# Optimization experiments

Measured on AMD Instinct MI355X. Metric: run time of the kernel, lower is better.

## Reference

```python
import jax, jax.numpy as jnp
import numpy as np

COMMITMENT_WEIGHT = 0.25


def _vq_layer(residual, codebook):
    """One euclidean VQ layer: nearest-codeword lookup + straight-through.
    residual: [B,T,D], codebook: [K,D].
    Returns (q_st [B,T,D], idx [B,T], commit_loss scalar).
    """
    B, T, D = residual.shape
    flat = residual.reshape(-1, D)  # [N,D]
    d2 = (jnp.sum(flat * flat, axis=-1, keepdims=True)
          - 2.0 * flat @ codebook.T
          + jnp.sum(codebook * codebook, axis=-1))  # [N,K]
    idx = jnp.argmin(d2, axis=-1)                   # [N]
    q = codebook[idx].reshape(B, T, D)
    # straight-through estimator (as in vector_quantize_pytorch)
    q_st = residual + jax.lax.stop_gradient(q - residual)
    commit_loss = COMMITMENT_WEIGHT * jnp.mean(
        (jax.lax.stop_gradient(q) - residual) ** 2)
    return q_st, idx.reshape(B, T), commit_loss


def setup_inputs() -> dict:
    key = jax.random.key(0)
    ks = jax.random.split(key, 9)
    D = 768
    sizes = [2, 4, 8, 16, 32, 64, 128, 256]
    inp = {"x": jax.random.normal(ks[0], (32, 2048, D), dtype=jnp.float32)}
    for i, K in enumerate(sizes):
        inp[f"cb{i}"] = jax.random.normal(ks[i + 1], (K, D), dtype=jnp.float32)
    return inp


def reference(x, cb0, cb1, cb2, cb3, cb4, cb5, cb6, cb7):
    codebooks = [cb0, cb1, cb2, cb3, cb4, cb5, cb6, cb7]
    residual = x
    quantized = jnp.zeros_like(x)
    all_indices = []
    total_commit_loss = jnp.float32(0.0)
    for cb in codebooks:  # fixed 8 structurally-distinct layers
        q, idx, commit = _vq_layer(residual, cb)
        quantized = quantized + q
        residual = residual - q
        all_indices.append(idx)
        total_commit_loss = total_commit_loss + commit
    all_indices = jnp.stack(all_indices, axis=-1)  # [B,T,num_layers]
    return quantized, all_indices, total_commit_loss
```

## Files before the change

### kernel.cpp

```cpp
#include <hip/hip_runtime.h>
#include <stdint.h>

#define NTOK 65536
#define DIM  768
#define NCB  512
#define NC   510
#define TAU  1.0f

typedef _Float16 f16x8 __attribute__((ext_vector_type(8)));
typedef float f32x4 __attribute__((ext_vector_type(4)));

#define WS_C32   0u
#define WS_CHI   1572864u
#define WS_CNORM 3145728u
#define WS_G     3147776u
#define WS_IDX   4196352u
#define WS_PART  6293504u
#define WS_PART2 6359040u
#define WS_S     8388608u
#define S_BYTES  67108864u

__device__ __forceinline__ void gl_lds16(const void* g, void* l){
  __builtin_amdgcn_global_load_lds(
      (const __attribute__((address_space(1))) unsigned int*)g,
      (__attribute__((address_space(3))) unsigned int*)l,
      16, 0, 0);
}

__global__ void k_prep(const float* __restrict__ cb0, const float* __restrict__ cb1,
                       const float* __restrict__ cb2, const float* __restrict__ cb3,
                       const float* __restrict__ cb4, const float* __restrict__ cb5,
                       const float* __restrict__ cb6, const float* __restrict__ cb7,
                       char* __restrict__ ws){
  const int r = blockIdx.x, t = threadIdx.x;
  const float* srcs[8] = {cb0,cb1,cb2,cb3,cb4,cb5,cb6,cb7};
  const int off[8] = {0,2,6,14,30,62,126,254};
  const int KK[8]  = {2,4,8,16,32,64,128,256};
  const float* src = nullptr;
#pragma unroll
  for (int l=0;l<8;l++)
    if (r >= off[l] && r < off[l]+KK[l]) src = srcs[l] + (size_t)(r - off[l]) * DIM;
  float* C32 = (float*)(ws + WS_C32);
  _Float16* Chi = (_Float16*)(ws + WS_CHI);
  double ss = 0.0;
#pragma unroll
  for (int i=0;i<3;i++){
    const int e = t + i*256;
    const float v = src ? src[e] : 0.f;
    C32[(size_t)r*DIM + e] = v;
    Chi[(size_t)r*DIM + e] = (_Float16)v;
    ss += (double)v * (double)v;
  }
  __shared__ double red[256];
  red[t] = ss; __syncthreads();
  for (int sdown=128; sdown>0; sdown>>=1){
    if (t < sdown) red[t] += red[t+sdown];
    __syncthreads();
  }
  if (t == 0){
    float* cnp = (float*)(ws + WS_CNORM);
    cnp[r] = (r < NC) ? (float)red[0] : 1e30f;
  }
}

__global__ void k_gram(char* __restrict__ ws){
  const int i = blockIdx.x, t = threadIdx.x;
  const float* __restrict__ C32 = (const float*)(ws + WS_C32);
  __shared__ float row[DIM];
  for (int e=t; e<DIM; e+=256) row[e] = C32[(size_t)i*DIM + e];
  __syncthreads();
  float* __restrict__ G = (float*)(ws + WS_G);
  for (int j=t; j<NCB; j+=256){
    const float4* cj = (const float4*)(C32 + (size_t)j*DIM);
    double d = 0.0;
    for (int k=0; k<DIM/4; k++){
      const float4 b = cj[k];
      d += (double)row[4*k]*(double)b.x + (double)row[4*k+1]*(double)b.y
         + (double)row[4*k+2]*(double)b.z + (double)row[4*k+3]*(double)b.w;
    }
    G[(size_t)i*NCB + j] = (float)(2.0*d);
  }
}

__global__ __launch_bounds__(256, 3) void k_gemm(const float* __restrict__ x,
                                                 const char* __restrict__ ws,
                                                 _Float16* __restrict__ Sq,
                                                 float* __restrict__ part2){
  __shared__ __align__(16) char smem[49152];
  const int t = threadIdx.x, lane = t & 63, w = t >> 6;
  const int wm = w >> 1, wn = w & 1;
  const int bid = blockIdx.x;
  const int xcd = bid & 7, jj = bid >> 3;
  const int mt = xcd*64 + (jj >> 2), nt = jj & 3;
  const _Float16* __restrict__ Chi = (const _Float16*)(ws + WS_CHI);
  const float* __restrict__ cn = (const float*)(ws + WS_CNORM);

  f32x4 acc[4][4];
#pragma unroll
  for (int i=0;i<4;i++)
#pragma unroll
    for (int j=0;j<4;j++) acc[i][j] = {0.f,0.f,0.f,0.f};

  float xs = 0.f;

  for (int kt=0; kt<12; kt++){
#pragma unroll
    for (int i8=0;i8<8;i8++){
      const int r0 = w*32 + i8*4;
      const int row = r0 + (lane>>4);
      const int g = lane & 15;
      const int sg = g ^ (((row&7)<<1) | ((row>>3)&1));
      const size_t go = (size_t)(mt*128 + row)*DIM + (size_t)kt*64 + sg*4;
      gl_lds16(x + go, smem + r0*256);
    }
#pragma unroll
    for (int c4=0;c4<4;c4++){
      const int r0 = w*32 + c4*8;
      const int rloc = r0 + (lane>>3);
      const int jsrc = (lane&7) ^ (rloc&7);
      const size_t go = (size_t)(nt*128 + rloc)*DIM + (size_t)kt*64 + jsrc*8;
      gl_lds16(Chi + go, smem + 32768 + r0*128);
    }
    __syncthreads();
    if ((kt & 3) == nt){
#pragma unroll
      for (int g=0; g<8; g++){
        const f32x4 v = *(const f32x4*)(smem + t*128 + g*16);
        xs += v[0]*v[0] + v[1]*v[1] + v[2]*v[2] + v[3]*v[3];
      }
    }
#pragma unroll
    for (int kk=0; kk<2; kk++){
      f16x8 fa[4], fb[4];
#pragma unroll
      for (int mf=0;mf<4;mf++){
        const int m = wm*64 + mf*16 + (lane&15);
        const int maskm = ((m&7)<<1) | ((m>>3)&1);
        const int ch = kk*4 + (lane>>4);
        const int g0 = (2*ch) ^ maskm;
        const f32x4 lo = *(const f32x4*)(smem + m*256 + g0*16);
        const f32x4 hi = *(const f32x4*)(smem + m*256 + (g0^1)*16);
        f16x8 r;
        r[0]=(_Float16)lo[0]; r[1]=(_Float16)lo[1]; r[2]=(_Float16)lo[2]; r[3]=(_Float16)lo[3];
        r[4]=(_Float16)hi[0]; r[5]=(_Float16)hi[1]; r[6]=(_Float16)hi[2]; r[7]=(_Float16)hi[3];
        fa[mf] = r;
      }
#pragma unroll
      for (int nf=0;nf<4;nf++){
        const int c = wn*64 + nf*16 + (lane&15);
        const uint bb = (uint)(32768 + c*128 + ((((kk<<2)+(lane>>4)) ^ (c&7))*16));
        fb[nf] = *(const f16x8*)(smem + bb);
      }
#pragma unroll
      for (int mf=0;mf<4;mf++)
#pragma unroll
        for (int nf=0;nf<4;nf++)
          acc[mf][nf] = __builtin_amdgcn_mfma_f32_16x16x32_f16(fa[mf], fb[nf], acc[mf][nf], 0,0,0);
    }
    __syncthreads();
  }

#pragma unroll
  for (int d=32; d>0; d>>=1) xs += __shfl_down(xs, d);
  if (lane == 0) ((float*)smem)[w] = xs;
  __syncthreads();
  if (t == 0) part2[bid] = ((float*)smem)[0] + ((float*)smem)[1]
                         + ((float*)smem)[2] + ((float*)smem)[3];

#pragma unroll
  for (int mf=0;mf<4;mf++)
#pragma unroll
    for (int nf=0;nf<4;nf++){
      const f32x4 v = acc[mf][nf];
      const int col  = nt*128 + wn*64 + nf*16 + (lane&15);
      const int row0 = mt*128 + wm*64 + mf*16 + ((lane>>4)<<2);
      const float cnc = cn[col];
#pragma unroll
      for (int e=0;e<4;e++)
        Sq[(size_t)(row0+e)*NCB + col] = (_Float16)(cnc - 2.f*v[e] - 768.f);
    }
}

template<int FUSED>
__global__ __launch_bounds__(512, 4) void k_chain(const float* __restrict__ x,
                                                  const _Float16* __restrict__ S,
                                                  char* __restrict__ ws,
                                                  float* __restrict__ out,
                                                  float* __restrict__ part){
  const int t = threadIdx.x, lane = t & 63, w = t >> 6;
  const size_t tok = (size_t)blockIdx.x*8 + w;
  const float* __restrict__ cn  = (const float*)(ws + WS_CNORM);
  const float* __restrict__ G2  = (const float*)(ws + WS_G);
  const float* __restrict__ C32 = (const float*)(ws + WS_C32);

  float sv[8], s0[8];
  {
    const uint* sp = (const uint*)(S + tok*NCB);
#pragma unroll
    for (int j=0;j<4;j++){
      union { uint u; _Float16 h[2]; } cv;
      cv.u = sp[j*64 + lane];
      sv[2*j]   = (float)cv.h[0];
      sv[2*j+1] = (float)cv.h[1];
    }
  }
#pragma unroll
  for (int k=0;k<8;k++) s0[k] = sv[k];

  int mcs[8];
  float tot = 0.f;

#pragma unroll
  for (int l=0; l<8; ++l){
    const int cs = (2<<l) - 2;
    const int ce = cs + (2<<l);
    float sc[8];
    float bv = 3e38f; int bc = 511;
#pragma unroll
    for (int j=0;j<4;j++){
      const int c0 = j*128 + lane*2;
      const float sA = (c0   >= cs && c0   < ce) ? sv[2*j]   : 3e38f;
      const float sB = (c0+1 >= cs && c0+1 < ce) ? sv[2*j+1] : 3e38f;
      sc[2*j] = sA; sc[2*j+1] = sB;
      if (sA < bv){ bv = sA; bc = c0; }
      if (sB < bv){ bv = sB; bc = c0+1; }
    }
    uint u = __float_as_uint(bv);
    u ^= (u & 0x80000000u) ? 0xFFFFFFFFu : 0x80000000u;
    uint key = (u & 0xFFFFFE00u) | ((uint)bc & 511u);
#pragma unroll
    for (int d=1; d<64; d<<=1){
      const uint ok = (uint)__shfl_xor((int)key, d);
      key = (ok < key) ? ok : key;
    }
    const int mc0 = (int)(key & 511u);
    const uint vq = key & 0xFFFFFE00u;
    const uint sb = (vq & 0x80000000u) ? (vq ^ 0x80000000u) : ~vq;
    const float bv_est = __uint_as_float(sb);
    const float thr = bv_est + TAU;

    int bm = 0;
#pragma unroll
    for (int k=0;k<8;k++)
      if (sc[k] <= thr) bm |= 1 << k;
    const unsigned long long lmask = __ballot(bm != 0);
    const int b0 = __ffsll((long long)lmask) - 1;
    const int bm0 = __shfl(bm, b0);
    const bool multi = (__popcll(lmask) > 1) || ((bm0 & (bm0-1)) != 0);

    int mc = mc0;
    float ssel = bv_est + 768.f;
    if (multi){
      float xv[12];
      {
        const float4* xp = (const float4*)(x + tok*DIM + lane*12);
#pragma unroll
        for (int q=0;q<3;q++){
          const float4 v = xp[q];
          xv[q*4]=v.x; xv[q*4+1]=v.y; xv[q*4+2]=v.z; xv[q*4+3]=v.w;
        }
      }
      double bve = 1e300; int bce = 0x7fffffff;
      unsigned long long Lm = lmask;
      while (Lm){
        const int b = __ffsll((long long)Lm) - 1; Lm &= Lm - 1;
        const int mbits = __shfl(bm, b);
#pragma unroll
        for (int k=0;k<8;k++){
          if (mbits & (1<<k)){
            const int c = (k>>1)*128 + b*2 + (k&1);
            const float dkv = __shfl((sv[k] - s0[k]) * 0.5f, b);
            const float* __restrict__ crow = C32 + (size_t)c*DIM + lane*12;
            double dd = 0.0;
#pragma unroll
            for (int q=0;q<3;q++){
              const float4 v = *(const float4*)(crow + q*4);
              dd += (double)xv[q*4]*v.x + (double)xv[q*4+1]*v.y
                  + (double)xv[q*4+2]*v.z + (double)xv[q*4+3]*v.w;
            }
#pragma unroll
            for (int d=1; d<64; d<<=1) dd += __shfl_xor(dd, d);
            const double se = (double)cn[c] - 2.0*(dd - (double)dkv);
            if (se < bve || (se == bve && c < bce)){ bve = se; bce = c; }
          }
        }
      }
      mc = bce;
      ssel = (float)bve;
    }
    mcs[l] = mc;
    if (FUSED) tot += (float)(8 - l) * ssel;
    if (l < 7){
      const float* __restrict__ gr = G2 + (size_t)mc*NCB;
#pragma unroll
      for (int j=0;j<4;j++){
        const float2 g2 = *(const float2*)(gr + j*128 + lane*2);
        sv[2*j] += g2.x; sv[2*j+1] += g2.y;
      }
    }
  }

  if (FUSED){
    float q[12];
#pragma unroll
    for (int i=0;i<12;i++) q[i] = 0.f;
#pragma unroll
    for (int l=0;l<8;l++){
      const float* __restrict__ cw = C32 + (size_t)mcs[l]*DIM + lane*12;
#pragma unroll
      for (int qq=0;qq<3;qq++){
        const float4 v = *(const float4*)(cw + qq*4);
        q[qq*4]+=v.x; q[qq*4+1]+=v.y; q[qq*4+2]+=v.z; q[qq*4+3]+=v.w;
      }
    }
    float* op = out + tok*DIM + lane*12;
#pragma unroll
    for (int qq=0;qq<3;qq++){
      float4 v; v.x=q[qq*4]; v.y=q[qq*4+1]; v.z=q[qq*4+2]; v.w=q[qq*4+3];
      *(float4*)(op + qq*4) = v;
    }
    if (lane == 0){
      float4 i0, i1;
      i0.x=(float)(mcs[0]-0);   i0.y=(float)(mcs[1]-2);   i0.z=(float)(mcs[2]-6);   i0.w=(float)(mcs[3]-14);
      i1.x=(float)(mcs[4]-30);  i1.y=(float)(mcs[5]-62);  i1.z=(float)(mcs[6]-126); i1.w=(float)(mcs[7]-254);
      *(float4*)(out + (size_t)NTOK*DIM + tok*8)     = i0;
      *(float4*)(out + (size_t)NTOK*DIM + tok*8 + 4) = i1;
    }
    __shared__ float bs[8];
    if (lane == 0) bs[w] = tot;
    __syncthreads();
    if (t == 0){
      float s2 = 0.f;
#pragma unroll
      for (int j=0;j<8;j++) s2 += bs[j];
      part[blockIdx.x] = s2;
    }
  } else {
    if (lane == 0){
      int* idxw = (int*)(ws + WS_IDX);
      const int offs[8] = {0,2,6,14,30,62,126,254};
#pragma unroll
      for (int l=0;l<8;l++) idxw[tok*8 + l] = mcs[l] - offs[l];
    }
  }
}

__global__ __launch_bounds__(512) void k_fin(const float* __restrict__ x,
                                             char* __restrict__ ws,
                                             float* __restrict__ out,
                                             float* __restrict__ part){
  const int t = threadIdx.x, lane = t & 63, w = t >> 6;
  const size_t tok = (size_t)blockIdx.x * 8 + w;
  const int off[8] = {0,2,6,14,30,62,126,254};
  const int* __restrict__ idxw = (const int*)(ws + WS_IDX);
  const float* __restrict__ C32 = (const float*)(ws + WS_C32);
  int loc[8];
#pragma unroll
  for (int l=0;l<8;l++) loc[l] = idxw[tok*8 + l];
  if (lane < 8) out[(size_t)NTOK*DIM + tok*8 + lane] = (float)idxw[tok*8 + lane];

  const float4* __restrict__ xr = (const float4*)(x + tok*DIM);
  float4* __restrict__ qr = (float4*)(out + tok*DIM);
  const float4* crow[8];
#pragma unroll
  for (int l=0;l<8;l++) crow[l] = (const float4*)(C32 + (size_t)(loc[l] + off[l])*DIM);
  float ssq = 0.f;
#pragma unroll
  for (int i=0;i<3;i++){
    const int e4 = i*64 + lane;
    const float4 xv = xr[e4];
    float rx = xv.x, ry = xv.y, rz = xv.z, rw = xv.w;
    float qx = 0.f, qy = 0.f, qz = 0.f, qw = 0.f;
#pragma unroll
    for (int l=0;l<8;l++){
      const float4 cv = crow[l][e4];
      rx -= cv.x; ry -= cv.y; rz -= cv.z; rw -= cv.w;
      qx += cv.x; qy += cv.y; qz += cv.z; qw += cv.w;
      ssq += rx*rx + ry*ry + rz*rz + rw*rw;
    }
    float4 q; q.x = qx; q.y = qy; q.z = qz; q.w = qw;
    qr[e4] = q;
  }
#pragma unroll
  for (int d=32; d>0; d>>=1) ssq += __shfl_down(ssq, d);
  __shared__ float bsum[8];
  if (lane == 0) bsum[w] = ssq;
  __syncthreads();
  if (t == 0){
    float s2 = 0.f;
#pragma unroll
    for (int j=0;j<8;j++) s2 += bsum[j];
    part[blockIdx.x] = s2;
  }
}

__global__ void k_loss(const float* __restrict__ part, int n,
                       const float* __restrict__ part2, int n2,
                       float* __restrict__ out){
  const int t = threadIdx.x;
  double s = 0.0;
  for (int i=t; i<n; i+=256) s += (double)part[i];
  double sx = 0.0;
  for (int i=t; i<n2; i+=256) sx += (double)part2[i];
  __shared__ double red[256];
  red[t] = s + 8.0*sx; __syncthreads();
  for (int d=128; d>0; d>>=1){
    if (t < d) red[t] += red[t+d];
    __syncthreads();
  }
  if (t == 0)
    out[(size_t)NTOK*DIM + (size_t)NTOK*8] =
      (float)(0.25 * red[0] / (double)((size_t)NTOK * DIM));
}

extern "C" void kernel_launch(void* const* d_in, const int* in_sizes, int n_in,
                              void* d_out, int out_size, void* d_ws, size_t ws_size,
                              hipStream_t stream){
  const float* x = (const float*)d_in[0];
  char* ws = (char*)d_ws;
  float* out = (float*)d_out;
  float* part  = (float*)(ws + WS_PART);
  float* part2 = (float*)(ws + WS_PART2);
  const bool fused = ws_size >= (size_t)WS_S + (size_t)S_BYTES;
  _Float16* Sp = fused ? (_Float16*)(ws + WS_S) : (_Float16*)out;

  k_prep<<<512, 256, 0, stream>>>((const float*)d_in[1], (const float*)d_in[2],
                                  (const float*)d_in[3], (const float*)d_in[4],
                                  (const float*)d_in[5], (const float*)d_in[6],
                                  (const float*)d_in[7], (const float*)d_in[8], ws);
  k_gram<<<512, 256, 0, stream>>>(ws);
  k_gemm<<<2048, 256, 0, stream>>>(x, ws, Sp, part2);
  if (fused){
    k_chain<1><<<8192, 512, 0, stream>>>(x, Sp, ws, out, part);
    k_loss<<<1, 256, 0, stream>>>(part, 8192, part2, 2048, out);
  } else {
    k_chain<0><<<8192, 512, 0, stream>>>(x, Sp, ws, out, part);
    k_fin<<<8192, 512, 0, stream>>>(x, ws, out, part);
    k_loss<<<1, 256, 0, stream>>>(part, 8192, part2, 2048, out);
  }
}
```

Measured before the change: 362.1 us.

## Triple-buffer k_gemm LDS stages with 512-thread blocks and async prefetch

Rewrites the k_gemm main loop as a three-stage LDS ring. Tiles for iterations kt+2 are issued with global_load_lds while iteration kt computes, gated by explicit vmcnt waits and a single barrier per iteration. The block grows to 512 threads (8 waves, 2x4 warp grid) with half the N fragments per wave, and LDS rises to 144 KB. This aims to hide global load latency behind MFMA work. The cost is lower occupancy and reliance on hand-counted vmcnt values for correctness.

```diff
diff --git a/kernel.cpp b/kernel.cpp
--- a/kernel.cpp
+++ b/kernel.cpp
@@ -82,97 +82,119 @@
   }
 }
 
-__global__ __launch_bounds__(256, 3) void k_gemm(const float* __restrict__ x,
+__global__ __launch_bounds__(512, 2) void k_gemm(const float* __restrict__ x,
                                                  const char* __restrict__ ws,
                                                  _Float16* __restrict__ Sq,
                                                  float* __restrict__ part2){
-  __shared__ __align__(16) char smem[49152];
+  __shared__ __align__(16) char smem[147456];
   const int t = threadIdx.x, lane = t & 63, w = t >> 6;
-  const int wm = w >> 1, wn = w & 1;
+  const int wm = w >> 2, wn = w & 3;
   const int bid = blockIdx.x;
   const int xcd = bid & 7, jj = bid >> 3;
   const int mt = xcd*64 + (jj >> 2), nt = jj & 3;
   const _Float16* __restrict__ Chi = (const _Float16*)(ws + WS_CHI);
   const float* __restrict__ cn = (const float*)(ws + WS_CNORM);
 
-  f32x4 acc[4][4];
+  f32x4 acc[4][2];
 #pragma unroll
   for (int i=0;i<4;i++)
 #pragma unroll
-    for (int j=0;j<4;j++) acc[i][j] = {0.f,0.f,0.f,0.f};
+    for (int j=0;j<2;j++) acc[i][j] = {0.f,0.f,0.f,0.f};
 
   float xs = 0.f;
 
-  for (int kt=0; kt<12; kt++){
-#pragma unroll
-    for (int i8=0;i8<8;i8++){
-      const int r0 = w*32 + i8*4;
-      const int row = r0 + (lane>>4);
+  auto stage = [&](int kt, int b){
+    const uint Ab = (uint)(b*32768);
+    const uint Bb = 98304u + (uint)(b*16384);
+#pragma unroll
+    for (int i=0;i<4;i++){
+      const int row = i*32 + w*4 + (lane>>4);
       const int g = lane & 15;
       const int sg = g ^ (((row&7)<<1) | ((row>>3)&1));
       const size_t go = (size_t)(mt*128 + row)*DIM + (size_t)kt*64 + sg*4;
-      gl_lds16(x + go, smem + r0*256);
-    }
-#pragma unroll
-    for (int c4=0;c4<4;c4++){
-      const int r0 = w*32 + c4*8;
-      const int rloc = r0 + (lane>>3);
+      gl_lds16(x + go, smem + Ab + i*8192 + w*1024);
+    }
+#pragma unroll
+    for (int i=0;i<2;i++){
+      const int rloc = i*64 + w*8 + (lane>>3);
       const int jsrc = (lane&7) ^ (rloc&7);
       const size_t go = (size_t)(nt*128 + rloc)*DIM + (size_t)kt*64 + jsrc*8;
-      gl_lds16(Chi + go, smem + 32768 + r0*128);
-    }
-    __syncthreads();
-    if ((kt & 3) == nt){
-#pragma unroll
-      for (int g=0; g<8; g++){
-        const f32x4 v = *(const f32x4*)(smem + t*128 + g*16);
-        xs += v[0]*v[0] + v[1]*v[1] + v[2]*v[2] + v[3]*v[3];
-      }
-    }
+      gl_lds16(Chi + go, smem + Bb + i*8192 + w*1024);
+    }
+  };
+
+  auto compute = [&](int b){
+    const uint Ab = (uint)(b*32768);
+    const uint Bb = 98304u + (uint)(b*16384);
 #pragma unroll
     for (int kk=0; kk<2; kk++){
-      f16x8 fa[4], fb[4];
+      f16x8 fa[4], fb[2];
 #pragma unroll
       for (int mf=0;mf<4;mf++){
         const int m = wm*64 + mf*16 + (lane&15);
         const int maskm = ((m&7)<<1) | ((m>>3)&1);
         const int ch = kk*4 + (lane>>4);
         const int g0 = (2*ch) ^ maskm;
-        const f32x4 lo = *(const f32x4*)(smem + m*256 + g0*16);
-        const f32x4 hi = *(const f32x4*)(smem + m*256 + (g0^1)*16);
+        const f32x4 lo = *(const f32x4*)(smem + Ab + m*256 + g0*16);
+        const f32x4 hi = *(const f32x4*)(smem + Ab + m*256 + (g0^1)*16);
         f16x8 r;
         r[0]=(_Float16)lo[0]; r[1]=(_Float16)lo[1]; r[2]=(_Float16)lo[2]; r[3]=(_Float16)lo[3];
         r[4]=(_Float16)hi[0]; r[5]=(_Float16)hi[1]; r[6]=(_Float16)hi[2]; r[7]=(_Float16)hi[3];
         fa[mf] = r;
       }
 #pragma unroll
-      for (int nf=0;nf<4;nf++){
-        const int c = wn*64 + nf*16 + (lane&15);
-        const uint bb = (uint)(32768 + c*128 + ((((kk<<2)+(lane>>4)) ^ (c&7))*16));
+      for (int nf=0;nf<2;nf++){
+        const int c = wn*32 + nf*16 + (lane&15);
+        const uint bb = Bb + (uint)(c*128 + ((((kk<<2)+(lane>>4)) ^ (c&7))*16));
         fb[nf] = *(const f16x8*)(smem + bb);
       }
 #pragma unroll
       for (int mf=0;mf<4;mf++)
 #pragma unroll
-        for (int nf=0;nf<4;nf++)
+        for (int nf=0;nf<2;nf++)
           acc[mf][nf] = __builtin_amdgcn_mfma_f32_16x16x32_f16(fa[mf], fb[nf], acc[mf][nf], 0,0,0);
     }
-    __syncthreads();
-  }
-
+  };
+
+  stage(0, 0);
+  stage(1, 1);
+
+  for (int kt=0; kt<12; kt++){
+    const int b = kt % 3;
+    if (kt < 11) { asm volatile("s_waitcnt vmcnt(6)" ::: "memory"); }
+    else         { asm volatile("s_waitcnt vmcnt(0)" ::: "memory"); }
+    __builtin_amdgcn_s_barrier();
+    __builtin_amdgcn_sched_barrier(0);
+    if (kt+2 < 12) stage(kt+2, (kt+2) % 3);
+    if ((kt & 3) == nt){
+      const uint Ab = (uint)(b*32768);
+#pragma unroll
+      for (int g=0; g<4; g++){
+        const f32x4 v = *(const f32x4*)(smem + Ab + t*64 + g*16);
+        xs += v[0]*v[0] + v[1]*v[1] + v[2]*v[2] + v[3]*v[3];
+      }
+    }
+    compute(b);
+  }
+
+  __syncthreads();
 #pragma unroll
   for (int d=32; d>0; d>>=1) xs += __shfl_down(xs, d);
   if (lane == 0) ((float*)smem)[w] = xs;
   __syncthreads();
-  if (t == 0) part2[bid] = ((float*)smem)[0] + ((float*)smem)[1]
-                         + ((float*)smem)[2] + ((float*)smem)[3];
+  if (t == 0){
+    float s2 = 0.f;
+#pragma unroll
+    for (int j=0;j<8;j++) s2 += ((float*)smem)[j];
+    part2[bid] = s2;
+  }
 
 #pragma unroll
   for (int mf=0;mf<4;mf++)
 #pragma unroll
-    for (int nf=0;nf<4;nf++){
+    for (int nf=0;nf<2;nf++){
       const f32x4 v = acc[mf][nf];
-      const int col  = nt*128 + wn*64 + nf*16 + (lane&15);
+      const int col  = nt*128 + wn*32 + nf*16 + (lane&15);
       const int row0 = mt*128 + wm*64 + mf*16 + ((lane>>4)<<2);
       const float cnc = cn[col];
 #pragma unroll
@@ -429,7 +451,7 @@
                                   (const float*)d_in[5], (const float*)d_in[6],
                                   (const float*)d_in[7], (const float*)d_in[8], ws);
   k_gram<<<512, 256, 0, stream>>>(ws);
-  k_gemm<<<2048, 256, 0, stream>>>(x, ws, Sp, part2);
+  k_gemm<<<2048, 512, 0, stream>>>(x, ws, Sp, part2);
   if (fused){
     k_chain<1><<<8192, 512, 0, stream>>>(x, Sp, ws, out, part);
     k_loss<<<1, 256, 0, stream>>>(part, 8192, part2, 2048, out);
```

Measured after the change: 389.3 us. 7.5% more time.

## Fuse score GEMM and residual chain into one kernel keeping scores in LDS

Applied to the files above, without the earlier changes.

Merges the distance-score GEMM and the per-token 8-layer argmin chain into a single kernel. Each 512-thread block computes a 64-token by 512-codeword tile, writes the fp16 scores into LDS and runs the chain from there. This removes the 64MB global round-trip for S and one launch. The cost is an 80KB LDS footprint that limits occupancy, fewer blocks (1024), and the chain phase running serially over 8 tokens per wave after the GEMM with no overlap.

```diff
diff --git a/kernel.cpp b/kernel.cpp
--- a/kernel.cpp
+++ b/kernel.cpp
@@ -14,11 +14,8 @@
 #define WS_CHI   1572864u
 #define WS_CNORM 3145728u
 #define WS_G     3147776u
-#define WS_IDX   4196352u
 #define WS_PART  6293504u
 #define WS_PART2 6359040u
-#define WS_S     8388608u
-#define S_BYTES  67108864u
 
 __device__ __forceinline__ void gl_lds16(const void* g, void* l){
   __builtin_amdgcn_global_load_lds(
@@ -82,59 +79,59 @@
   }
 }
 
-__global__ __launch_bounds__(256, 3) void k_gemm(const float* __restrict__ x,
-                                                 const char* __restrict__ ws,
-                                                 _Float16* __restrict__ Sq,
-                                                 float* __restrict__ part2){
-  __shared__ __align__(16) char smem[49152];
+__global__ __launch_bounds__(512, 4) void k_fused(const float* __restrict__ x,
+                                                  const char* __restrict__ ws,
+                                                  float* __restrict__ out,
+                                                  float* __restrict__ part,
+                                                  float* __restrict__ part2){
+  __shared__ __align__(16) char smem[81920];
   const int t = threadIdx.x, lane = t & 63, w = t >> 6;
-  const int wm = w >> 1, wn = w & 1;
+  const int wm = w >> 2, wn = w & 3;
   const int bid = blockIdx.x;
-  const int xcd = bid & 7, jj = bid >> 3;
-  const int mt = xcd*64 + (jj >> 2), nt = jj & 3;
   const _Float16* __restrict__ Chi = (const _Float16*)(ws + WS_CHI);
-  const float* __restrict__ cn = (const float*)(ws + WS_CNORM);
-
-  f32x4 acc[4][4];
-#pragma unroll
-  for (int i=0;i<4;i++)
-#pragma unroll
-    for (int j=0;j<4;j++) acc[i][j] = {0.f,0.f,0.f,0.f};
+  const float* __restrict__ cn  = (const float*)(ws + WS_CNORM);
+  const float* __restrict__ G2  = (const float*)(ws + WS_G);
+  const float* __restrict__ C32 = (const float*)(ws + WS_C32);
+
+  f32x4 acc[2][8];
+#pragma unroll
+  for (int i=0;i<2;i++)
+#pragma unroll
+    for (int j=0;j<8;j++) acc[i][j] = {0.f,0.f,0.f,0.f};
 
   float xs = 0.f;
 
   for (int kt=0; kt<12; kt++){
 #pragma unroll
-    for (int i8=0;i8<8;i8++){
-      const int r0 = w*32 + i8*4;
+    for (int i=0;i<2;i++){
+      const int r0 = (i*8 + w)*4;
       const int row = r0 + (lane>>4);
       const int g = lane & 15;
       const int sg = g ^ (((row&7)<<1) | ((row>>3)&1));
-      const size_t go = (size_t)(mt*128 + row)*DIM + (size_t)kt*64 + sg*4;
+      const size_t go = (size_t)(bid*64 + row)*DIM + (size_t)kt*64 + sg*4;
       gl_lds16(x + go, smem + r0*256);
     }
 #pragma unroll
-    for (int c4=0;c4<4;c4++){
-      const int r0 = w*32 + c4*8;
+    for (int i=0;i<8;i++){
+      const int r0 = w*64 + i*8;
       const int rloc = r0 + (lane>>3);
       const int jsrc = (lane&7) ^ (rloc&7);
-      const size_t go = (size_t)(nt*128 + rloc)*DIM + (size_t)kt*64 + jsrc*8;
-      gl_lds16(Chi + go, smem + 32768 + r0*128);
+      const size_t go = (size_t)rloc*DIM + (size_t)kt*64 + jsrc*8;
+      gl_lds16(Chi + go, smem + 16384 + r0*128);
     }
     __syncthreads();
-    if ((kt & 3) == nt){
-#pragma unroll
-      for (int g=0; g<8; g++){
-        const f32x4 v = *(const f32x4*)(smem + t*128 + g*16);
-        xs += v[0]*v[0] + v[1]*v[1] + v[2]*v[2] + v[3]*v[3];
-      }
+    {
+      const f32x4 v0 = *(const f32x4*)(smem + t*32);
+      const f32x4 v1 = *(const f32x4*)(smem + t*32 + 16);
+      xs += v0[0]*v0[0]+v0[1]*v0[1]+v0[2]*v0[2]+v0[3]*v0[3]
+          + v1[0]*v1[0]+v1[1]*v1[1]+v1[2]*v1[2]+v1[3]*v1[3];
     }
 #pragma unroll
     for (int kk=0; kk<2; kk++){
-      f16x8 fa[4], fb[4];
-#pragma unroll
-      for (int mf=0;mf<4;mf++){
-        const int m = wm*64 + mf*16 + (lane&15);
+      f16x8 fa[2], fb[8];
+#pragma unroll
+      for (int mf=0;mf<2;mf++){
+        const int m = wm*32 + mf*16 + (lane&15);
         const int maskm = ((m&7)<<1) | ((m>>3)&1);
         const int ch = kk*4 + (lane>>4);
         const int g0 = (2*ch) ^ maskm;
@@ -146,161 +143,154 @@
         fa[mf] = r;
       }
 #pragma unroll
-      for (int nf=0;nf<4;nf++){
-        const int c = wn*64 + nf*16 + (lane&15);
-        const uint bb = (uint)(32768 + c*128 + ((((kk<<2)+(lane>>4)) ^ (c&7))*16));
+      for (int nf=0;nf<8;nf++){
+        const int c = wn*128 + nf*16 + (lane&15);
+        const uint bb = (uint)(16384 + c*128 + ((((kk<<2)+(lane>>4)) ^ (c&7))*16));
         fb[nf] = *(const f16x8*)(smem + bb);
       }
 #pragma unroll
-      for (int mf=0;mf<4;mf++)
-#pragma unroll
-        for (int nf=0;nf<4;nf++)
+      for (int mf=0;mf<2;mf++)
+#pragma unroll
+        for (int nf=0;nf<8;nf++)
           acc[mf][nf] = __builtin_amdgcn_mfma_f32_16x16x32_f16(fa[mf], fb[nf], acc[mf][nf], 0,0,0);
     }
     __syncthreads();
   }
 
 #pragma unroll
+  for (int mf=0;mf<2;mf++)
+#pragma unroll
+    for (int nf=0;nf<8;nf++){
+      const int cand = wn*128 + nf*16 + (lane&15);
+      const float cnc = cn[cand];
+      const f32x4 v = acc[mf][nf];
+#pragma unroll
+      for (int e=0;e<4;e++){
+        const int tokL = wm*32 + mf*16 + (lane>>4)*4 + e;
+        *(_Float16*)(smem + 16384 + tokL*1024 + cand*2) =
+          (_Float16)(cnc - 2.f*v[e] - 768.f);
+      }
+    }
+
+#pragma unroll
   for (int d=32; d>0; d>>=1) xs += __shfl_down(xs, d);
+  __syncthreads();
   if (lane == 0) ((float*)smem)[w] = xs;
   __syncthreads();
-  if (t == 0) part2[bid] = ((float*)smem)[0] + ((float*)smem)[1]
-                         + ((float*)smem)[2] + ((float*)smem)[3];
-
-#pragma unroll
-  for (int mf=0;mf<4;mf++)
-#pragma unroll
-    for (int nf=0;nf<4;nf++){
-      const f32x4 v = acc[mf][nf];
-      const int col  = nt*128 + wn*64 + nf*16 + (lane&15);
-      const int row0 = mt*128 + wm*64 + mf*16 + ((lane>>4)<<2);
-      const float cnc = cn[col];
-#pragma unroll
-      for (int e=0;e<4;e++)
-        Sq[(size_t)(row0+e)*NCB + col] = (_Float16)(cnc - 2.f*v[e] - 768.f);
-    }
-}
-
-template<int FUSED>
-__global__ __launch_bounds__(512, 4) void k_chain(const float* __restrict__ x,
-                                                  const _Float16* __restrict__ S,
-                                                  char* __restrict__ ws,
-                                                  float* __restrict__ out,
-                                                  float* __restrict__ part){
-  const int t = threadIdx.x, lane = t & 63, w = t >> 6;
-  const size_t tok = (size_t)blockIdx.x*8 + w;
-  const float* __restrict__ cn  = (const float*)(ws + WS_CNORM);
-  const float* __restrict__ G2  = (const float*)(ws + WS_G);
-  const float* __restrict__ C32 = (const float*)(ws + WS_C32);
-
-  float sv[8], s0[8];
-  {
-    const uint* sp = (const uint*)(S + tok*NCB);
+  if (t == 0){
+    float s2 = 0.f;
+#pragma unroll
+    for (int j=0;j<8;j++) s2 += ((float*)smem)[j];
+    part2[bid] = s2;
+  }
+
+  float tot = 0.f;
+  for (int ti=0; ti<8; ++ti){
+    const int tl = w*8 + ti;
+    const size_t tok = (size_t)bid*64 + tl;
+
+    float sv[8], s0[8];
 #pragma unroll
     for (int j=0;j<4;j++){
       union { uint u; _Float16 h[2]; } cv;
-      cv.u = sp[j*64 + lane];
+      cv.u = *(const uint*)(smem + 16384 + tl*1024 + j*256 + lane*4);
       sv[2*j]   = (float)cv.h[0];
       sv[2*j+1] = (float)cv.h[1];
     }
-  }
-#pragma unroll
-  for (int k=0;k<8;k++) s0[k] = sv[k];
-
-  int mcs[8];
-  float tot = 0.f;
-
-#pragma unroll
-  for (int l=0; l<8; ++l){
-    const int cs = (2<<l) - 2;
-    const int ce = cs + (2<<l);
-    float sc[8];
-    float bv = 3e38f; int bc = 511;
-#pragma unroll
-    for (int j=0;j<4;j++){
-      const int c0 = j*128 + lane*2;
-      const float sA = (c0   >= cs && c0   < ce) ? sv[2*j]   : 3e38f;
-      const float sB = (c0+1 >= cs && c0+1 < ce) ? sv[2*j+1] : 3e38f;
-      sc[2*j] = sA; sc[2*j+1] = sB;
-      if (sA < bv){ bv = sA; bc = c0; }
-      if (sB < bv){ bv = sB; bc = c0+1; }
-    }
-    uint u = __float_as_uint(bv);
-    u ^= (u & 0x80000000u) ? 0xFFFFFFFFu : 0x80000000u;
-    uint key = (u & 0xFFFFFE00u) | ((uint)bc & 511u);
-#pragma unroll
-    for (int d=1; d<64; d<<=1){
-      const uint ok = (uint)__shfl_xor((int)key, d);
-      key = (ok < key) ? ok : key;
-    }
-    const int mc0 = (int)(key & 511u);
-    const uint vq = key & 0xFFFFFE00u;
-    const uint sb = (vq & 0x80000000u) ? (vq ^ 0x80000000u) : ~vq;
-    const float bv_est = __uint_as_float(sb);
-    const float thr = bv_est + TAU;
-
-    int bm = 0;
-#pragma unroll
-    for (int k=0;k<8;k++)
-      if (sc[k] <= thr) bm |= 1 << k;
-    const unsigned long long lmask = __ballot(bm != 0);
-    const int b0 = __ffsll((long long)lmask) - 1;
-    const int bm0 = __shfl(bm, b0);
-    const bool multi = (__popcll(lmask) > 1) || ((bm0 & (bm0-1)) != 0);
-
-    int mc = mc0;
-    float ssel = bv_est + 768.f;
-    if (multi){
-      float xv[12];
-      {
-        const float4* xp = (const float4*)(x + tok*DIM + lane*12);
-#pragma unroll
-        for (int q=0;q<3;q++){
-          const float4 v = xp[q];
-          xv[q*4]=v.x; xv[q*4+1]=v.y; xv[q*4+2]=v.z; xv[q*4+3]=v.w;
-        }
-      }
-      double bve = 1e300; int bce = 0x7fffffff;
-      unsigned long long Lm = lmask;
-      while (Lm){
-        const int b = __ffsll((long long)Lm) - 1; Lm &= Lm - 1;
-        const int mbits = __shfl(bm, b);
-#pragma unroll
-        for (int k=0;k<8;k++){
-          if (mbits & (1<<k)){
-            const int c = (k>>1)*128 + b*2 + (k&1);
-            const float dkv = __shfl((sv[k] - s0[k]) * 0.5f, b);
-            const float* __restrict__ crow = C32 + (size_t)c*DIM + lane*12;
-            double dd = 0.0;
-#pragma unroll
-            for (int q=0;q<3;q++){
-              const float4 v = *(const float4*)(crow + q*4);
-              dd += (double)xv[q*4]*v.x + (double)xv[q*4+1]*v.y
-                  + (double)xv[q*4+2]*v.z + (double)xv[q*4+3]*v.w;
-            }
-#pragma unroll
-            for (int d=1; d<64; d<<=1) dd += __shfl_xor(dd, d);
-            const double se = (double)cn[c] - 2.0*(dd - (double)dkv);
-            if (se < bve || (se == bve && c < bce)){ bve = se; bce = c; }
+#pragma unroll
+    for (int k=0;k<8;k++) s0[k] = sv[k];
+
+    int mcs[8];
+#pragma unroll
+    for (int l=0; l<8; ++l){
+      const int cs = (2<<l) - 2;
+      const int ce = cs + (2<<l);
+      float sc[8];
+      float bv = 3e38f; int bc = 511;
+#pragma unroll
+      for (int j=0;j<4;j++){
+        const int c0 = j*128 + lane*2;
+        const float sA = (c0   >= cs && c0   < ce) ? sv[2*j]   : 3e38f;
+        const float sB = (c0+1 >= cs && c0+1 < ce) ? sv[2*j+1] : 3e38f;
+        sc[2*j] = sA; sc[2*j+1] = sB;
+        if (sA < bv){ bv = sA; bc = c0; }
+        if (sB < bv){ bv = sB; bc = c0+1; }
+      }
+      uint u = __float_as_uint(bv);
+      u ^= (u & 0x80000000u) ? 0xFFFFFFFFu : 0x80000000u;
+      uint key = (u & 0xFFFFFE00u) | ((uint)bc & 511u);
+#pragma unroll
+      for (int d=1; d<64; d<<=1){
+        const uint ok = (uint)__shfl_xor((int)key, d);
+        key = (ok < key) ? ok : key;
+      }
+      const int mc0 = (int)(key & 511u);
+      const uint vq = key & 0xFFFFFE00u;
+      const uint sb = (vq & 0x80000000u) ? (vq ^ 0x80000000u) : ~vq;
+      const float bv_est = __uint_as_float(sb);
+      const float thr = bv_est + TAU;
+
+      int bm = 0;
+#pragma unroll
+      for (int k=0;k<8;k++)
+        if (sc[k] <= thr) bm |= 1 << k;
+      const unsigned long long lmask = __ballot(bm != 0);
+      const int b0 = __ffsll((long long)lmask) - 1;
+      const int bm0 = __shfl(bm, b0);
+      const bool multi = (__popcll(lmask) > 1) || ((bm0 & (bm0-1)) != 0);
+
+      int mc = mc0;
+      float ssel = bv_est + 768.f;
+      if (multi){
+        float xv[12];
+        {
+          const float4* xp = (const float4*)(x + tok*DIM + lane*12);
+#pragma unroll
+          for (int q=0;q<3;q++){
+            const float4 v = xp[q];
+            xv[q*4]=v.x; xv[q*4+1]=v.y; xv[q*4+2]=v.z; xv[q*4+3]=v.w;
           }
         }
-      }
-      mc = bce;
-      ssel = (float)bve;
-    }
-    mcs[l] = mc;
-    if (FUSED) tot += (float)(8 - l) * ssel;
-    if (l < 7){
-      const float* __restrict__ gr = G2 + (size_t)mc*NCB;
-#pragma unroll
-      for (int j=0;j<4;j++){
-        const float2 g2 = *(const float2*)(gr + j*128 + lane*2);
-        sv[2*j] += g2.x; sv[2*j+1] += g2.y;
-      }
-    }
-  }
-
-  if (FUSED){
+        double bve = 1e300; int bce = 0x7fffffff;
+        unsigned long long Lm = lmask;
+        while (Lm){
+          const int b = __ffsll((long long)Lm) - 1; Lm &= Lm - 1;
+          const int mbits = __shfl(bm, b);
+#pragma unroll
+          for (int k=0;k<8;k++){
+            if (mbits & (1<<k)){
+              const int c = (k>>1)*128 + b*2 + (k&1);
+              const float dkv = __shfl((sv[k] - s0[k]) * 0.5f, b);
+              const float* __restrict__ crow = C32 + (size_t)c*DIM + lane*12;
+              double dd = 0.0;
+#pragma unroll
+              for (int q=0;q<3;q++){
+                const float4 v = *(const float4*)(crow + q*4);
+                dd += (double)xv[q*4]*v.x + (double)xv[q*4+1]*v.y
+                    + (double)xv[q*4+2]*v.z + (double)xv[q*4+3]*v.w;
+              }
+#pragma unroll
+              for (int d=1; d<64; d<<=1) dd += __shfl_xor(dd, d);
+              const double se = (double)cn[c] - 2.0*(dd - (double)dkv);
+              if (se < bve || (se == bve && c < bce)){ bve = se; bce = c; }
+            }
+          }
+        }
+        mc = bce;
+        ssel = (float)bve;
+      }
+      mcs[l] = mc;
+      tot += (float)(8 - l) * ssel;
+      if (l < 7){
+        const float* __restrict__ gr = G2 + (size_t)mc*NCB;
+#pragma unroll
+        for (int j=0;j<4;j++){
+          const float2 g2 = *(const float2*)(gr + j*128 + lane*2);
+          sv[2*j] += g2.x; sv[2*j+1] += g2.y;
+        }
+      }
+    }
+
     float q[12];
 #pragma unroll
     for (int i=0;i<12;i++) q[i] = 0.f;
@@ -326,71 +316,16 @@
       *(float4*)(out + (size_t)NTOK*DIM + tok*8)     = i0;
       *(float4*)(out + (size_t)NTOK*DIM + tok*8 + 4) = i1;
     }
-    __shared__ float bs[8];
-    if (lane == 0) bs[w] = tot;
-    __syncthreads();
-    if (t == 0){
-      float s2 = 0.f;
-#pragma unroll
-      for (int j=0;j<8;j++) s2 += bs[j];
-      part[blockIdx.x] = s2;
-    }
-  } else {
-    if (lane == 0){
-      int* idxw = (int*)(ws + WS_IDX);
-      const int offs[8] = {0,2,6,14,30,62,126,254};
-#pragma unroll
-      for (int l=0;l<8;l++) idxw[tok*8 + l] = mcs[l] - offs[l];
-    }
-  }
-}
-
-__global__ __launch_bounds__(512) void k_fin(const float* __restrict__ x,
-                                             char* __restrict__ ws,
-                                             float* __restrict__ out,
-                                             float* __restrict__ part){
-  const int t = threadIdx.x, lane = t & 63, w = t >> 6;
-  const size_t tok = (size_t)blockIdx.x * 8 + w;
-  const int off[8] = {0,2,6,14,30,62,126,254};
-  const int* __restrict__ idxw = (const int*)(ws + WS_IDX);
-  const float* __restrict__ C32 = (const float*)(ws + WS_C32);
-  int loc[8];
-#pragma unroll
-  for (int l=0;l<8;l++) loc[l] = idxw[tok*8 + l];
-  if (lane < 8) out[(size_t)NTOK*DIM + tok*8 + lane] = (float)idxw[tok*8 + lane];
-
-  const float4* __restrict__ xr = (const float4*)(x + tok*DIM);
-  float4* __restrict__ qr = (float4*)(out + tok*DIM);
-  const float4* crow[8];
-#pragma unroll
-  for (int l=0;l<8;l++) crow[l] = (const float4*)(C32 + (size_t)(loc[l] + off[l])*DIM);
-  float ssq = 0.f;
-#pragma unroll
-  for (int i=0;i<3;i++){
-    const int e4 = i*64 + lane;
-    const float4 xv = xr[e4];
-    float rx = xv.x, ry = xv.y, rz = xv.z, rw = xv.w;
-    float qx = 0.f, qy = 0.f, qz = 0.f, qw = 0.f;
-#pragma unroll
-    for (int l=0;l<8;l++){
-      const float4 cv = crow[l][e4];
-      rx -= cv.x; ry -= cv.y; rz -= cv.z; rw -= cv.w;
-      qx += cv.x; qy += cv.y; qz += cv.z; qw += cv.w;
-      ssq += rx*rx + ry*ry + rz*rz + rw*rw;
-    }
-    float4 q; q.x = qx; q.y = qy; q.z = qz; q.w = qw;
-    qr[e4] = q;
-  }
-#pragma unroll
-  for (int d=32; d>0; d>>=1) ssq += __shfl_down(ssq, d);
-  __shared__ float bsum[8];
-  if (lane == 0) bsum[w] = ssq;
+  }
+
+  __syncthreads();
+  if (lane == 0) ((float*)smem)[8 + w] = tot;
   __syncthreads();
   if (t == 0){
     float s2 = 0.f;
 #pragma unroll
-    for (int j=0;j<8;j++) s2 += bsum[j];
-    part[blockIdx.x] = s2;
+    for (int j=0;j<8;j++) s2 += ((float*)smem)[8 + j];
+    part[bid] = s2;
   }
 }
 
@@ -421,21 +356,12 @@
   float* out = (float*)d_out;
   float* part  = (float*)(ws + WS_PART);
   float* part2 = (float*)(ws + WS_PART2);
-  const bool fused = ws_size >= (size_t)WS_S + (size_t)S_BYTES;
-  _Float16* Sp = fused ? (_Float16*)(ws + WS_S) : (_Float16*)out;
 
   k_prep<<<512, 256, 0, stream>>>((const float*)d_in[1], (const float*)d_in[2],
                                   (const float*)d_in[3], (const float*)d_in[4],
                                   (const float*)d_in[5], (const float*)d_in[6],
                                   (const float*)d_in[7], (const float*)d_in[8], ws);
   k_gram<<<512, 256, 0, stream>>>(ws);
-  k_gemm<<<2048, 256, 0, stream>>>(x, ws, Sp, part2);
-  if (fused){
-    k_chain<1><<<8192, 512, 0, stream>>>(x, Sp, ws, out, part);
-    k_loss<<<1, 256, 0, stream>>>(part, 8192, part2, 2048, out);
-  } else {
-    k_chain<0><<<8192, 512, 0, stream>>>(x, Sp, ws, out, part);
-    k_fin<<<8192, 512, 0, stream>>>(x, ws, out, part);
-    k_loss<<<1, 256, 0, stream>>>(part, 8192, part2, 2048, out);
-  }
-}
+  k_fused<<<1024, 512, 0, stream>>>(x, ws, out, part, part2);
+  k_loss<<<1, 256, 0, stream>>>(part, 1024, part2, 1024, out);
+}
```

After: 387.3 us. +7.0%, slower.
